# Kernel tuning notes

Measured on AMD Instinct MI355X. Metric: run time of the kernel, lower is better.

## Reference

```python
import jax, jax.numpy as jnp
import numpy as np

B, S, D = 4, 2048, 2048  # batch, seq, input_dim == state_dim
N = D

def setup_inputs() -> dict:
    key = jax.random.key(0)
    ks = jax.random.split(key, 6)
    x = jax.random.normal(ks[0], (B, S, D), dtype=jnp.float32)
    W_dt = jax.random.normal(ks[1], (N, D), dtype=jnp.float32) / np.sqrt(D)
    b_dt = jnp.ones((N,), dtype=jnp.float32)  # dt_proj.bias.fill_(1.0)
    W_B = jax.random.normal(ks[2], (N, D), dtype=jnp.float32) / np.sqrt(D)
    W_C = jax.random.normal(ks[3], (D, N), dtype=jnp.float32) / np.sqrt(N)
    A_log = jax.random.normal(ks[4], (N,), dtype=jnp.float32) * 0.5 - 1.0
    D_skip = jnp.zeros((D,), dtype=jnp.float32)
    return {"x": x, "W_dt": W_dt, "b_dt": b_dt, "W_B": W_B, "W_C": W_C,
            "A_log": A_log, "D_skip": D_skip}

def reference(x, W_dt, b_dt, W_B, W_C, A_log, D_skip):
    # dt = softplus(x @ W_dt^T + b_dt) -> [B,S,N]
    dt = jax.nn.softplus(jnp.einsum('bsd,nd->bsn', x, W_dt) + b_dt)
    Bp = jnp.einsum('bsd,nd->bsn', x, W_B)          # [B,S,N]
    A = -jnp.exp(A_log)                              # [N]
    A_bar = jnp.exp(dt * A)                          # [B,S,N]
    inputs = (dt * Bp) * x                           # B_bar * x (N == D)
    # selective scan: h_t = A_bar_t * h_{t-1} + inputs_t
    h0 = jnp.zeros((x.shape[0], A_log.shape[0]), dtype=x.dtype)
    def step(h, ab_u):
        ab, u = ab_u
        h = ab * h + u
        return h, h
    # scan over time axis: move S to leading axis
    _, h_all = jax.lax.scan(step, h0,
                            (jnp.swapaxes(A_bar, 0, 1), jnp.swapaxes(inputs, 0, 1)))
    h_all = jnp.swapaxes(h_all, 0, 1)                # [B,S,N]
    out = jnp.einsum('bsn,dn->bsd', h_all, W_C) + D_skip * x
    return out
```

## Files before the change

kernel.cpp:

```cpp
#include <hip/hip_runtime.h>

#define SEQ    2048
#define DIM    2048
#define NBATCH 4
#define MTOT   (NBATCH * SEQ)
#define CHUNKS 32
#define CLEN   (SEQ / CHUNKS)
#define CSH    5
#define HT_ELEMS (256 * 32)

typedef __bf16 bf16_t;
typedef __bf16 bf16x8 __attribute__((ext_vector_type(8)));
typedef float  f32x4  __attribute__((ext_vector_type(4)));
typedef unsigned short u16x4 __attribute__((ext_vector_type(4)));
typedef unsigned short u16x2 __attribute__((ext_vector_type(2)));

typedef __attribute__((address_space(3))) bf16_t lds_bf16;

__device__ __forceinline__ unsigned short f2bf_rne(float f) {
    unsigned int u = __float_as_uint(f);
    u += 0x7fffu + ((u >> 16) & 1u);
    return (unsigned short)(u >> 16);
}
__device__ __forceinline__ float bf2f(unsigned short v) {
    return __uint_as_float((unsigned int)v << 16);
}

__global__ void k_prep_all(const float* __restrict__ x, const float* __restrict__ W_dt,
                           const float* __restrict__ W_B, const float* __restrict__ W_C,
                           const float* __restrict__ A_log,
                           unsigned short* __restrict__ xb, unsigned short* __restrict__ wcat,
                           unsigned short* __restrict__ wcb, float* __restrict__ negA) {
    const int n4x = MTOT * DIM / 4;
    const int n4w = DIM * DIM / 4;
    int i = blockIdx.x * blockDim.x + threadIdx.x;
    if (i < n4x) {
        f32x4 v = ((const f32x4*)x)[i];
        u16x4 o;
        o[0] = f2bf_rne(v[0]); o[1] = f2bf_rne(v[1]);
        o[2] = f2bf_rne(v[2]); o[3] = f2bf_rne(v[3]);
        ((u16x4*)xb)[i] = o;
        return;
    }
    i -= n4x;
    if (i < 2 * n4w) {
        int phase = (i >= n4w);
        int j = phase ? i - n4w : i;
        const float* src = phase ? W_B : W_dt;
        const int R4 = DIM / 4;
        int nrow = j / R4;
        int dcol = j - nrow * R4;
        f32x4 v = ((const f32x4*)src)[j];
        u16x4 o;
        o[0] = f2bf_rne(v[0]); o[1] = f2bf_rne(v[1]);
        o[2] = f2bf_rne(v[2]); o[3] = f2bf_rne(v[3]);
        ((u16x4*)wcat)[(2 * nrow + phase) * R4 + dcol] = o;
        return;
    }
    i -= 2 * n4w;
    if (i < n4w) {
        f32x4 v = ((const f32x4*)W_C)[i];
        u16x4 o;
        o[0] = f2bf_rne(v[0]); o[1] = f2bf_rne(v[1]);
        o[2] = f2bf_rne(v[2]); o[3] = f2bf_rne(v[3]);
        ((u16x4*)wcb)[i] = o;
        return;
    }
    i -= n4w;
    if (i < DIM / 4) {
        f32x4 v = ((const f32x4*)A_log)[i];
        f32x4 o;
        o[0] = -__expf(v[0]); o[1] = -__expf(v[1]);
        o[2] = -__expf(v[2]); o[3] = -__expf(v[3]);
        ((f32x4*)negA)[i] = o;
    }
}

__device__ __forceinline__ void stage_half(const bf16_t* __restrict__ gbase, int K,
                                           int k0, char* ldsbase) {
#pragma unroll
    for (int q = 0; q < 2; q++) {
        __builtin_amdgcn_global_load_lds(
            (const __attribute__((address_space(1))) void*)(gbase + (long)q * 16 * K + k0),
            (__attribute__((address_space(3))) void*)(ldsbase + q * 1024),
            16, 0, 0);
    }
}

#define MFMA_B16(a, b, c) __builtin_amdgcn_mfma_f32_16x16x32_bf16(a, b, c, 0, 0, 0)
#define BAR  __builtin_amdgcn_s_barrier()
#define SBAR __builtin_amdgcn_sched_barrier(0)
#define DSR(D, P) asm volatile("ds_read_b128 %0, %1" : "=v"(D) : "v"(P))

template <int KTILES>
__device__ __forceinline__ void gemm256_main(const bf16_t* __restrict__ A,
                                             const bf16_t* __restrict__ Bm,
                                             int K, long arow0, long brow0,
                                             bf16_t* As, bf16_t* Bs,
                                             f32x4 acc[8][4],
                                             int wave, int lane, int wm, int wn) {
    const int l15  = lane & 15;
    const int quad = lane >> 4;
    const int swz  = (quad ^ ((l15 >> 1) & 3)) * 8;
    const int aoff = (wm * 128 + l15) * 32 + swz;
    const int boff = (wn * 64  + l15) * 32 + swz;

    const lds_bf16* Aw = ((const lds_bf16*)As) + aoff;
    const lds_bf16* Bw = ((const lds_bf16*)Bs) + boff;

    const int rl     = lane >> 2;
    const int gchunk = (lane & 3) ^ ((lane >> 3) & 3);
    const bf16_t* gA = A  + (arow0 + wave * 32 + rl) * (long)K + gchunk * 8;
    const bf16_t* gB = Bm + (brow0 + wave * 32 + rl) * (long)K + gchunk * 8;
    char* ldsA = (char*)As + wave * 2048;
    char* ldsB = (char*)Bs + wave * 2048;

    auto stA = [&](int buf, int ks, int kt) {
        stage_half(gA, K, kt * 64 + ks * 32, ldsA + (buf * 2 + ks) * (HT_ELEMS * 2));
    };
    auto stB = [&](int buf, int ks, int kt) {
        stage_half(gB, K, kt * 64 + ks * 32, ldsB + (buf * 2 + ks) * (HT_ELEMS * 2));
    };

    stB(0, 0, 0); stA(0, 0, 0); stB(0, 1, 0); stA(0, 1, 0);
    stB(1, 0, 1); stA(1, 0, 1); stB(1, 1, 1);
    asm volatile("s_waitcnt vmcnt(6)");
    SBAR;
    BAR;

    bf16x8 a0, a1, a2, a3, b0, b1, b2, b3;

#define LDAB03(BUF, KS) { \
    const lds_bf16* pa = Aw + ((BUF) * 2 + (KS)) * HT_ELEMS; \
    const lds_bf16* pb = Bw + ((BUF) * 2 + (KS)) * HT_ELEMS; \
    DSR(a0, pa);        DSR(b0, pb); \
    DSR(a1, pa + 512);  DSR(b1, pb + 512); \
    DSR(a2, pa + 1024); DSR(b2, pb + 1024); \
    DSR(a3, pa + 1536); DSR(b3, pb + 1536); }
#define LDA47(BUF, KS) { \
    const lds_bf16* pa = Aw + ((BUF) * 2 + (KS)) * HT_ELEMS + 2048; \
    DSR(a0, pa); DSR(a1, pa + 512); DSR(a2, pa + 1024); DSR(a3, pa + 1536); }
#define MM16(I0) \
    SBAR; \
    BAR; \
    asm volatile("s_waitcnt lgkmcnt(0)"); \
    SBAR; \
    __builtin_amdgcn_s_setprio(1); \
    acc[(I0)+0][0] = MFMA_B16(a0, b0, acc[(I0)+0][0]); \
    acc[(I0)+0][1] = MFMA_B16(a0, b1, acc[(I0)+0][1]); \
    acc[(I0)+0][2] = MFMA_B16(a0, b2, acc[(I0)+0][2]); \
    acc[(I0)+0][3] = MFMA_B16(a0, b3, acc[(I0)+0][3]); \
    acc[(I0)+1][0] = MFMA_B16(a1, b0, acc[(I0)+1][0]); \
    acc[(I0)+1][1] = MFMA_B16(a1, b1, acc[(I0)+1][1]); \
    acc[(I0)+1][2] = MFMA_B16(a1, b2, acc[(I0)+1][2]); \
    acc[(I0)+1][3] = MFMA_B16(a1, b3, acc[(I0)+1][3]); \
    acc[(I0)+2][0] = MFMA_B16(a2, b0, acc[(I0)+2][0]); \
    acc[(I0)+2][1] = MFMA_B16(a2, b1, acc[(I0)+2][1]); \
    acc[(I0)+2][2] = MFMA_B16(a2, b2, acc[(I0)+2][2]); \
    acc[(I0)+2][3] = MFMA_B16(a2, b3, acc[(I0)+2][3]); \
    acc[(I0)+3][0] = MFMA_B16(a3, b0, acc[(I0)+3][0]); \
    acc[(I0)+3][1] = MFMA_B16(a3, b1, acc[(I0)+3][1]); \
    acc[(I0)+3][2] = MFMA_B16(a3, b2, acc[(I0)+3][2]); \
    acc[(I0)+3][3] = MFMA_B16(a3, b3, acc[(I0)+3][3]); \
    __builtin_amdgcn_s_setprio(0); \
    SBAR; \
    BAR;

#pragma unroll 1
    for (int t = 0; t < KTILES / 2; ++t) {
        const bool nlast = (t != KTILES / 2 - 1);
        const int k1 = 2 * t + 1, k2 = 2 * t + 2, k3 = 2 * t + 3;
        LDAB03(0, 0);
        stA(1, 1, k1);
        MM16(0);
        LDA47(0, 0);
        if (nlast) stB(0, 0, k2);
        MM16(4);
        LDAB03(0, 1);
        if (nlast) stA(0, 0, k2);
        MM16(0);
        LDA47(0, 1);
        if (nlast) stB(0, 1, k2);
        if (nlast) { asm volatile("s_waitcnt vmcnt(6)"); }
        else       { asm volatile("s_waitcnt vmcnt(0)"); }
        MM16(4);
        LDAB03(1, 0);
        if (nlast) stA(0, 1, k2);
        MM16(0);
        LDA47(1, 0);
        if (nlast) stB(1, 0, k3);
        MM16(4);
        LDAB03(1, 1);
        if (nlast) stA(1, 0, k3);
        MM16(0);
        LDA47(1, 1);
        if (nlast) stB(1, 1, k3);
        if (nlast) { asm volatile("s_waitcnt vmcnt(6)"); }
        MM16(4);
    }
#undef LDAB03
#undef LDA47
#undef MM16
}

__global__ __launch_bounds__(512, 2)
void k_gemm_fused(const bf16_t* __restrict__ A, const bf16_t* __restrict__ Wcat,
                  const float* __restrict__ x, const float* __restrict__ b_dt,
                  const float* __restrict__ negA,
                  unsigned short* __restrict__ abuf, unsigned short* __restrict__ ubuf) {
    __shared__ __align__(16) bf16_t As[4 * HT_ELEMS];
    __shared__ __align__(16) bf16_t Bs[4 * HT_ELEMS];

    const int tid  = threadIdx.x;
    const int lane = tid & 63;
    const int wave = tid >> 6;
    const int wm   = wave >> 2;
    const int wn   = wave & 3;
    int flat = blockIdx.x;
    int swzb = (flat & 7) * 64 + (flat >> 3);
    int bm = swzb & 31;
    int bn = swzb >> 5;

    f32x4 acc[8][4];
#pragma unroll
    for (int i = 0; i < 8; i++)
#pragma unroll
        for (int j = 0; j < 4; j++) acc[i][j] = (f32x4){0.f, 0.f, 0.f, 0.f};

    gemm256_main<DIM / 64>(A, Wcat, DIM, (long)bm * 256, (long)bn * 256,
                           As, Bs, acc, wave, lane, wm, wn);

    const int l15  = lane & 15;
    const int quad = lane >> 4;
    const int odd  = l15 & 1;
#pragma unroll
    for (int i = 0; i < 8; i++) {
#pragma unroll
        for (int j = 0; j < 4; j++) {
#pragma unroll
            for (int r = 0; r < 4; r++) {
                float v = acc[i][j][r];
                float w = __shfl_xor(v, 1);
                float dtpre = odd ? w : v;
                float bpv   = odd ? v : w;
                long row = (long)bm * 256 + wm * 128 + i * 16 + quad * 4 + r;
                int  col = bn * 256 + wn * 64 + j * 16 + l15;
                int  n   = col >> 1;
                float z  = dtpre + b_dt[n];
                float dt = (z > 15.f) ? z : __logf(1.f + __expf(z));
                float a  = __expf(negA[n] * dt);
                float u  = dt * bpv * x[row * DIM + n];
                long idx = row * DIM + n;
                if (odd) ubuf[idx] = f2bf_rne(u); else abuf[idx] = f2bf_rne(a);
            }
        }
    }
}

__global__ __launch_bounds__(512, 2)
void k_gemm_bt(const bf16_t* __restrict__ A, const bf16_t* __restrict__ Bm,
               float* __restrict__ C, int N, int K,
               const float* __restrict__ skip, const float* __restrict__ xres) {
    __shared__ __align__(16) bf16_t As[4 * HT_ELEMS];
    __shared__ __align__(16) bf16_t Bs[4 * HT_ELEMS];

    const int tid  = threadIdx.x;
    const int lane = tid & 63;
    const int wave = tid >> 6;
    const int wm   = wave >> 2;
    const int wn   = wave & 3;
    int flat = blockIdx.x;
    int swzb = (flat & 7) * 32 + (flat >> 3);
    int bm = swzb & 31;
    int bn = swzb >> 5;

    f32x4 acc[8][4];
#pragma unroll
    for (int i = 0; i < 8; i++)
#pragma unroll
        for (int j = 0; j < 4; j++) acc[i][j] = (f32x4){0.f, 0.f, 0.f, 0.f};

    gemm256_main<DIM / 64>(A, Bm, K, (long)bm * 256, (long)bn * 256,
                           As, Bs, acc, wave, lane, wm, wn);

    const int l15  = lane & 15;
    const int quad = lane >> 4;
#pragma unroll
    for (int i = 0; i < 8; i++) {
#pragma unroll
        for (int j = 0; j < 4; j++) {
#pragma unroll
            for (int r = 0; r < 4; r++) {
                long row = (long)bm * 256 + wm * 128 + i * 16 + quad * 4 + r;
                long col = (long)bn * 256 + wn * 64 + j * 16 + l15;
                long idx = row * (long)N + col;
                float v = acc[i][j][r];
                if (skip) v += skip[col] * xres[idx];
                C[idx] = v;
            }
        }
    }
}

__global__ void k_scan1(const unsigned short* __restrict__ a,
                        const unsigned short* __restrict__ u,
                        float* __restrict__ P, float* __restrict__ V) {
    int t  = blockIdx.x * blockDim.x + threadIdx.x;
    int n2 = t & (DIM / 2 - 1);
    int c  = (t >> 10) & (CHUNKS - 1);
    int b  = t >> (10 + CSH);
    long base = ((long)b * SEQ + (long)c * CLEN) * DIM + n2 * 2;
    float p0 = 1.f, v0 = 0.f, p1 = 1.f, v1 = 0.f;
    for (int s = 0; s < CLEN; s++) {
        u16x2 av = *(const u16x2*)(a + base + (long)s * DIM);
        u16x2 uv = *(const u16x2*)(u + base + (long)s * DIM);
        float a0 = bf2f(av[0]), a1 = bf2f(av[1]);
        v0 = a0 * v0 + bf2f(uv[0]);  p0 *= a0;
        v1 = a1 * v1 + bf2f(uv[1]);  p1 *= a1;
    }
    long pidx = ((long)b * CHUNKS + c) * DIM + n2 * 2;
    *(float2*)(P + pidx) = make_float2(p0, p1);
    *(float2*)(V + pidx) = make_float2(v0, v1);
}

__global__ void k_scan2(const float* __restrict__ P, const float* __restrict__ V,
                        float* __restrict__ carry) {
    int t = blockIdx.x * blockDim.x + threadIdx.x;
    int n = t & (DIM - 1);
    int b = t >> 11;
    float H = 0.f;
    for (int c = 0; c < CHUNKS; c++) {
        long idx = ((long)b * CHUNKS + c) * DIM + n;
        carry[idx] = H;
        H = P[idx] * H + V[idx];
    }
}

__global__ void k_scan3(const unsigned short* __restrict__ a,
                        const unsigned short* __restrict__ u,
                        const float* __restrict__ carry,
                        unsigned short* __restrict__ h) {
    int t  = blockIdx.x * blockDim.x + threadIdx.x;
    int n2 = t & (DIM / 2 - 1);
    int c  = (t >> 10) & (CHUNKS - 1);
    int b  = t >> (10 + CSH);
    long base = ((long)b * SEQ + (long)c * CLEN) * DIM + n2 * 2;
    long cidx = ((long)b * CHUNKS + c) * DIM + n2 * 2;
    float2 Hc = *(const float2*)(carry + cidx);
    float H0 = Hc.x, H1 = Hc.y;
    for (int s = 0; s < CLEN; s++) {
        u16x2 av = *(const u16x2*)(a + base + (long)s * DIM);
        u16x2 uv = *(const u16x2*)(u + base + (long)s * DIM);
        H0 = bf2f(av[0]) * H0 + bf2f(uv[0]);
        H1 = bf2f(av[1]) * H1 + bf2f(uv[1]);
        u16x2 o; o[0] = f2bf_rne(H0); o[1] = f2bf_rne(H1);
        *(u16x2*)(h + base + (long)s * DIM) = o;
    }
}

extern "C" void kernel_launch(void* const* d_in, const int* in_sizes, int n_in,
                              void* d_out, int out_size, void* d_ws, size_t ws_size,
                              hipStream_t stream) {
    const float* x      = (const float*)d_in[0];
    const float* W_dt   = (const float*)d_in[1];
    const float* b_dt   = (const float*)d_in[2];
    const float* W_B    = (const float*)d_in[3];
    const float* W_C    = (const float*)d_in[4];
    const float* A_log  = (const float*)d_in[5];
    const float* D_skip = (const float*)d_in[6];
    float* out = (float*)d_out;

    char* ws = (char*)d_ws;
    size_t off = 0;
    auto alloc = [&](size_t bytes) -> char* {
        char* p = ws + off;
        off += (bytes + 255) & ~(size_t)255;
        return p;
    };
    unsigned short* xb   = (unsigned short*)alloc((size_t)MTOT * DIM * 2);
    unsigned short* wcat = (unsigned short*)alloc((size_t)2 * DIM * DIM * 2);
    unsigned short* wcb  = (unsigned short*)alloc((size_t)DIM * DIM * 2);
    unsigned short* abuf = (unsigned short*)alloc((size_t)MTOT * DIM * 2);
    unsigned short* ubuf = (unsigned short*)alloc((size_t)MTOT * DIM * 2);
    float* P     = (float*)alloc((size_t)NBATCH * CHUNKS * DIM * 4);
    float* V     = (float*)alloc((size_t)NBATCH * CHUNKS * DIM * 4);
    float* carry = (float*)alloc((size_t)NBATCH * CHUNKS * DIM * 4);
    float* negA  = (float*)alloc((size_t)DIM * 4);

    const int prep_threads = MTOT * DIM / 4 + 3 * (DIM * DIM / 4) + DIM / 4;
    k_prep_all<<<(prep_threads + 255) / 256, 256, 0, stream>>>(
        x, W_dt, W_B, W_C, A_log, xb, wcat, wcb, negA);

    k_gemm_fused<<<(MTOT / 256) * (2 * DIM / 256), 512, 0, stream>>>(
        (const bf16_t*)xb, (const bf16_t*)wcat, x, b_dt, negA, abuf, ubuf);

    const int scan_threads = NBATCH * CHUNKS * DIM / 2;
    k_scan1<<<scan_threads / 256, 256, 0, stream>>>(abuf, ubuf, P, V);
    k_scan2<<<(NBATCH * DIM) / 256, 256, 0, stream>>>(P, V, carry);
    k_scan3<<<scan_threads / 256, 256, 0, stream>>>(abuf, ubuf, carry, xb );

    k_gemm_bt<<<(MTOT / 256) * (DIM / 256), 512, 0, stream>>>(
        (const bf16_t*)xb, (const bf16_t*)wcb, out, DIM, DIM, D_skip, x);
}
```

Baseline: 489.0 us.

## Switch fused dt/B GEMM to 128x128 tiles with simple double-buffered main loop

Replaces the 256x256, 8-wave hand-pipelined GEMM in the fused dt/B-projection kernel with a 128x128 tile, 4-wave kernel that double-buffers 32-wide K slices in LDS and issues one barrier per iteration. The grid grows fourfold and the block-index swizzle for L2 locality becomes a plain column-major mapping. The intent is higher occupancy and better wave balance across CUs. The cost is lower arithmetic intensity per tile, more global/L2 traffic, and a less carefully interleaved load/MFMA schedule.

After: 549.5 us. +12.4%, slower.

```diff
diff --git a/kernel.cpp b/kernel.cpp
--- a/kernel.cpp
+++ b/kernel.cpp
@@ -7,6 +7,8 @@
 #define CHUNKS 32
 #define CLEN   (SEQ / CHUNKS)
 #define CSH    5
+#define NBM    (MTOT / 128)
+#define TILE128 (128 * 32)
 #define HT_ELEMS (256 * 32)
 
 typedef __bf16 bf16_t;
@@ -76,21 +78,65 @@
     }
 }
 
-__device__ __forceinline__ void stage_half(const bf16_t* __restrict__ gbase, int K,
-                                           int k0, char* ldsbase) {
-#pragma unroll
-    for (int q = 0; q < 2; q++) {
-        __builtin_amdgcn_global_load_lds(
-            (const __attribute__((address_space(1))) void*)(gbase + (long)q * 16 * K + k0),
-            (__attribute__((address_space(3))) void*)(ldsbase + q * 1024),
-            16, 0, 0);
-    }
-}
-
 #define MFMA_B16(a, b, c) __builtin_amdgcn_mfma_f32_16x16x32_bf16(a, b, c, 0, 0, 0)
 #define BAR  __builtin_amdgcn_s_barrier()
 #define SBAR __builtin_amdgcn_sched_barrier(0)
 #define DSR(D, P) asm volatile("ds_read_b128 %0, %1" : "=v"(D) : "v"(P))
+
+__device__ __forceinline__ void glds16(const bf16_t* g, char* l) {
+    __builtin_amdgcn_global_load_lds(
+        (const __attribute__((address_space(1))) void*)g,
+        (__attribute__((address_space(3))) void*)l, 16, 0, 0);
+}
+
+template <int KITERS>
+__device__ __forceinline__ void gemm_main128(const bf16_t* __restrict__ A,
+                                             const bf16_t* __restrict__ Bm,
+                                             int K, long arow0, long brow0,
+                                             bf16_t* As, bf16_t* Bs,
+                                             f32x4 acc[4][4],
+                                             int wave, int lane, int wm, int wn) {
+    const int l15  = lane & 15;
+    const int quad = lane >> 4;
+    const int swz  = (quad ^ ((l15 >> 1) & 3)) * 8;
+    const int rl     = lane >> 2;
+    const int gchunk = (lane & 3) ^ ((lane >> 3) & 3);
+
+    const bf16_t* gA0 = A  + (arow0 + wave * 32 + rl) * (long)K + gchunk * 8;
+    const bf16_t* gA1 = gA0 + 16 * (long)K;
+    const bf16_t* gB0 = Bm + (brow0 + wave * 32 + rl) * (long)K + gchunk * 8;
+    const bf16_t* gB1 = gB0 + 16 * (long)K;
+    char* ldsA = (char*)As + wave * 2048;
+    char* ldsB = (char*)Bs + wave * 2048;
+
+    auto stage = [&](int i) {
+        char* la = ldsA + (i & 1) * (TILE128 * 2);
+        char* lb = ldsB + (i & 1) * (TILE128 * 2);
+        const int k0 = i * 32;
+        glds16(gA0 + k0, la); glds16(gA1 + k0, la + 1024);
+        glds16(gB0 + k0, lb); glds16(gB1 + k0, lb + 1024);
+    };
+
+    stage(0);
+#pragma unroll 2
+    for (int i = 0; i < KITERS; ++i) {
+        asm volatile("s_waitcnt vmcnt(0)\n\ts_barrier" ::: "memory");
+        const bf16_t* ap = As + (i & 1) * TILE128;
+        const bf16_t* bp = Bs + (i & 1) * TILE128;
+        bf16x8 af[4], bfr[4];
+#pragma unroll
+        for (int t = 0; t < 4; t++) {
+            af[t]  = *(const bf16x8*)(ap + (wm * 64 + t * 16 + l15) * 32 + swz);
+            bfr[t] = *(const bf16x8*)(bp + (wn * 64 + t * 16 + l15) * 32 + swz);
+        }
+        if (i + 1 < KITERS) stage(i + 1);
+#pragma unroll
+        for (int t = 0; t < 4; t++)
+#pragma unroll
+            for (int j = 0; j < 4; j++)
+                acc[t][j] = MFMA_B16(af[t], bfr[j], acc[t][j]);
+    }
+}
 
 template <int KTILES>
 __device__ __forceinline__ void gemm256_main(const bf16_t* __restrict__ A,
@@ -116,10 +162,14 @@
     char* ldsB = (char*)Bs + wave * 2048;
 
     auto stA = [&](int buf, int ks, int kt) {
-        stage_half(gA, K, kt * 64 + ks * 32, ldsA + (buf * 2 + ks) * (HT_ELEMS * 2));
+        char* l = ldsA + (buf * 2 + ks) * (HT_ELEMS * 2);
+        const int k0 = kt * 64 + ks * 32;
+        glds16(gA + k0, l); glds16(gA + 16 * (long)K + k0, l + 1024);
     };
     auto stB = [&](int buf, int ks, int kt) {
-        stage_half(gB, K, kt * 64 + ks * 32, ldsB + (buf * 2 + ks) * (HT_ELEMS * 2));
+        char* l = ldsB + (buf * 2 + ks) * (HT_ELEMS * 2);
+        const int k0 = kt * 64 + ks * 32;
+        glds16(gB + k0, l); glds16(gB + 16 * (long)K + k0, l + 1024);
     };
 
     stB(0, 0, 0); stA(0, 0, 0); stB(0, 1, 0); stA(0, 1, 0);
@@ -203,38 +253,37 @@
 #undef MM16
 }
 
-__global__ __launch_bounds__(512, 2)
+__global__ __launch_bounds__(256)
 void k_gemm_fused(const bf16_t* __restrict__ A, const bf16_t* __restrict__ Wcat,
                   const float* __restrict__ x, const float* __restrict__ b_dt,
                   const float* __restrict__ negA,
                   unsigned short* __restrict__ abuf, unsigned short* __restrict__ ubuf) {
-    __shared__ __align__(16) bf16_t As[4 * HT_ELEMS];
-    __shared__ __align__(16) bf16_t Bs[4 * HT_ELEMS];
+    __shared__ __align__(16) bf16_t As[2 * TILE128];
+    __shared__ __align__(16) bf16_t Bs[2 * TILE128];
 
     const int tid  = threadIdx.x;
     const int lane = tid & 63;
     const int wave = tid >> 6;
-    const int wm   = wave >> 2;
-    const int wn   = wave & 3;
-    int flat = blockIdx.x;
-    int swzb = (flat & 7) * 64 + (flat >> 3);
-    int bm = swzb & 31;
-    int bn = swzb >> 5;
-
-    f32x4 acc[8][4];
-#pragma unroll
-    for (int i = 0; i < 8; i++)
+    const int wm   = wave >> 1;
+    const int wn   = wave & 1;
+    int flat = blockIdx.y * gridDim.x + blockIdx.x;
+    int bm = flat % NBM;
+    int bn = flat / NBM;
+
+    f32x4 acc[4][4];
+#pragma unroll
+    for (int i = 0; i < 4; i++)
 #pragma unroll
         for (int j = 0; j < 4; j++) acc[i][j] = (f32x4){0.f, 0.f, 0.f, 0.f};
 
-    gemm256_main<DIM / 64>(A, Wcat, DIM, (long)bm * 256, (long)bn * 256,
+    gemm_main128<DIM / 32>(A, Wcat, DIM, (long)bm * 128, (long)bn * 128,
                            As, Bs, acc, wave, lane, wm, wn);
 
     const int l15  = lane & 15;
     const int quad = lane >> 4;
     const int odd  = l15 & 1;
 #pragma unroll
-    for (int i = 0; i < 8; i++) {
+    for (int i = 0; i < 4; i++) {
 #pragma unroll
         for (int j = 0; j < 4; j++) {
 #pragma unroll
@@ -243,8 +292,8 @@
                 float w = __shfl_xor(v, 1);
                 float dtpre = odd ? w : v;
                 float bpv   = odd ? v : w;
-                long row = (long)bm * 256 + wm * 128 + i * 16 + quad * 4 + r;
-                int  col = bn * 256 + wn * 64 + j * 16 + l15;
+                long row = (long)bm * 128 + wm * 64 + i * 16 + quad * 4 + r;
+                int  col = bn * 128 + wn * 64 + j * 16 + l15;
                 int  n   = col >> 1;
                 float z  = dtpre + b_dt[n];
                 float dt = (z > 15.f) ? z : __logf(1.f + __expf(z));
@@ -391,8 +440,9 @@
     k_prep_all<<<(prep_threads + 255) / 256, 256, 0, stream>>>(
         x, W_dt, W_B, W_C, A_log, xb, wcat, wcb, negA);
 
-    k_gemm_fused<<<(MTOT / 256) * (2 * DIM / 256), 512, 0, stream>>>(
-        (const bf16_t*)xb, (const bf16_t*)wcat, x, b_dt, negA, abuf, ubuf);
+    dim3 fgrid(2 * DIM / 128, MTOT / 128);
+    k_gemm_fused<<<fgrid, 256, 0, stream>>>((const bf16_t*)xb, (const bf16_t*)wcat,
+                                            x, b_dt, negA, abuf, ubuf);
 
     const int scan_threads = NBATCH * CHUNKS * DIM / 2;
     k_scan1<<<scan_threads / 256, 256, 0, stream>>>(abuf, ubuf, P, V);
```
